# Kernel tuning notes

Hardware: AMD Instinct MI355X
Metric: run time of the kernel (lower is better)

## Reference

```python
import jax, jax.numpy as jnp
import numpy as np

G = 4          # groups
K = 3          # kernel_size
INC = 64       # channels


def conv3x3(x, w):
    # x: (B, Cin, H, W), w: (Cout, Cin, 3, 3), stride 1, pad 1, no bias
    return jax.lax.conv_general_dilated(
        x, w, window_strides=(1, 1), padding=[(1, 1), (1, 1)],
        dimension_numbers=("NCHW", "OIHW", "NCHW"))


def pconv(x, w):
    # partial conv: 3x3 conv on first C//4 channels, rest untouched
    dc = x.shape[1] // 4
    x1 = conv3x3(x[:, :dc], w)
    return jnp.concatenate([x1, x[:, dc:]], axis=1)


def conv1x1(x, w, b):
    # w: (Cout, Cin), b: (Cout,)
    return jnp.einsum("bchw,oc->bohw", x, w) + b[None, :, None, None]


def deform_sample(img, offset, mask_sig, dilation):
    """Modulated deformable sampling (DSMv3): for each output pixel and each of
    the K*K kernel taps, bilinearly sample img at p + dilated_tap + offset and
    modulate by the (sigmoided) mask. Returns (B, Cg, K*K, H, W)."""
    b, cg, H, W = img.shape
    K2 = K * K
    off = offset.reshape(b, K2, 2, H, W)  # (dy, dx) per tap
    ky = jnp.repeat(jnp.arange(K), K).astype(img.dtype)   # (K2,) row of tap
    kx = jnp.tile(jnp.arange(K), K).astype(img.dtype)     # (K2,) col of tap
    # padding = center*dilation so sampling grid is centered: p = i + (k-1)*dil
    base_y = jnp.arange(H, dtype=img.dtype)[None, :, None] + ((ky - 1.0) * dilation)[:, None, None]  # (K2,H,1)
    base_x = jnp.arange(W, dtype=img.dtype)[None, None, :] + ((kx - 1.0) * dilation)[:, None, None]  # (K2,1,W)
    py = base_y[None] + off[:, :, 0]  # (B,K2,H,W)
    px = base_x[None] + off[:, :, 1]  # (B,K2,H,W)

    y0 = jnp.floor(py)
    x0 = jnp.floor(px)
    wy = py - y0
    wx = px - x0
    imgf = img.reshape(b, cg, H * W)

    def corner(yi, xi, wgt):
        valid = ((yi >= 0) & (yi <= H - 1) & (xi >= 0) & (xi <= W - 1)).astype(img.dtype)
        yc = jnp.clip(yi, 0, H - 1).astype(jnp.int32)
        xc = jnp.clip(xi, 0, W - 1).astype(jnp.int32)
        flat = (yc * W + xc).reshape(b, 1, -1)  # (B,1,K2*H*W)
        v = jnp.take_along_axis(imgf, flat, axis=2).reshape(b, cg, K2, H, W)
        return v * (wgt * valid).reshape(b, 1, K2, H, W)

    val = (corner(y0, x0, (1 - wy) * (1 - wx))
           + corner(y0, x0 + 1, (1 - wy) * wx)
           + corner(y0 + 1, x0, wy * (1 - wx))
           + corner(y0 + 1, x0 + 1, wy * wx))
    return val * mask_sig[:, None]  # (B,Cg,K2,H,W)


def setup_inputs() -> dict:
    key = jax.random.key(0)
    ks = jax.random.split(key, 8)
    dc = INC // 4
    x = jax.random.normal(ks[0], (4, INC, 128, 128), dtype=jnp.float32)
    y = jax.random.normal(ks[1], (8, INC, 128, 128), dtype=jnp.float32)
    # learned params (small random so offsets stay near-zero, as after training warmup)
    offset_pconv_w = jax.random.normal(ks[2], (G, dc, dc, 3, 3), dtype=jnp.float32) * 0.1
    offset_w = jax.random.normal(ks[3], (G, 2 * K * K, INC), dtype=jnp.float32) * 0.1
    offset_b = jax.random.normal(ks[4], (G, 2 * K * K), dtype=jnp.float32) * 0.1
    mask_pconv_w = jax.random.normal(ks[5], (dc, dc, 3, 3), dtype=jnp.float32) * 0.1
    mask_w = jax.random.normal(ks[6], (K * K, INC), dtype=jnp.float32) * 0.1
    mask_b = jax.random.normal(ks[7], (K * K,), dtype=jnp.float32) * 0.1
    return {"x": x, "y": y,
            "offset_pconv_w": offset_pconv_w, "offset_w": offset_w, "offset_b": offset_b,
            "mask_pconv_w": mask_pconv_w, "mask_w": mask_w, "mask_b": mask_b}


def reference(x, y, offset_pconv_w, offset_w, offset_b, mask_pconv_w, mask_w, mask_b):
    b, c, h, w = x.shape
    cg = c // G
    mask = jax.nn.sigmoid(conv1x1(pconv(x, mask_pconv_w), mask_w, mask_b))  # (B,K2,H,W), shared
    y1, y2 = jnp.split(y, 2, axis=0)
    outs1, outs2 = [], []
    for g in range(G):
        offset = conv1x1(pconv(x, offset_pconv_w[g]), offset_w[g], offset_b[g])  # (B,2*K2,H,W)
        dil = 2 * g + 1
        outs1.append(deform_sample(y1[:, g * cg:(g + 1) * cg], offset, mask, dil))
        outs2.append(deform_sample(y2[:, g * cg:(g + 1) * cg], offset, mask, dil))
    y1n = jnp.concatenate(outs1, axis=1)  # (B,C,K2,H,W)
    y2n = jnp.concatenate(outs2, axis=1)
    return jnp.concatenate([y1n, y2n], axis=0)  # (2B,C,K2,H,W)
```

## Files before the change

### kernel.cpp

```cpp
#include <hip/hip_runtime.h>
#include <hip/hip_bf16.h>
#include <math.h>

constexpr int HH   = 128;
constexpr int WW   = 128;
constexpr int HWsz = HH * WW;

constexpr long OFFS_OFF = 0;
constexpr long MASK_OFF = OFFS_OFF + 4L * 4 * 18 * HWsz;
constexpr long WEO_OFF  = MASK_OFF + 4L * 9 * HWsz;
constexpr long WRO_OFF  = WEO_OFF + 4L * 16 * 9 * 18;
constexpr long WEM_OFF  = WRO_OFF + 4L * 48 * 18;
constexpr long WRM_OFF  = WEM_OFF + 16L * 9 * 9;
constexpr long YT_OFF   = WRM_OFF + 48L * 9;

__global__ __launch_bounds__(256) void prep_kernel(
    const float* __restrict__ off_pw,
    const float* __restrict__ off_w,
    const float* __restrict__ mask_pw,
    const float* __restrict__ mask_w,
    float* __restrict__ Weff_off, float* __restrict__ Wraw_off,
    float* __restrict__ Weff_mask, float* __restrict__ Wraw_mask)
{
    const int i = blockIdx.x * 256 + threadIdx.x;
    if (i < 10368) {
        const int o = i % 18; int r = i / 18;
        const int t = r % 9;  r /= 9;
        const int ci = r % 16; const int g = r / 16;
        float s = 0.f;
        for (int co = 0; co < 16; ++co)
            s += off_w[(g * 18 + o) * 64 + co] *
                 off_pw[((g * 16 + co) * 16 + ci) * 9 + t];
        Weff_off[i] = s;
    } else if (i < 10368 + 3456) {
        const int j = i - 10368;
        const int o = j % 18; int r = j / 18;
        const int c = r % 48; const int g = r / 48;
        Wraw_off[j] = off_w[(g * 18 + o) * 64 + 16 + c];
    } else if (i < 10368 + 3456 + 1296) {
        const int j = i - 13824;
        const int o = j % 9; int r = j / 9;
        const int t = r % 9; const int ci = r / 9;
        float s = 0.f;
        for (int co = 0; co < 16; ++co)
            s += mask_w[o * 64 + co] * mask_pw[((co * 16) + ci) * 9 + t];
        Weff_mask[j] = s;
    } else if (i < 10368 + 3456 + 1296 + 432) {
        const int j = i - 15120;
        const int o = j % 9; const int c = j / 9;
        Wraw_mask[j] = mask_w[o * 64 + 16 + c];
    }
}

__global__ __launch_bounds__(256) void transpose_kernel(
    const float* __restrict__ y, float* __restrict__ yT)
{
    __shared__ __align__(16) float tile[256][20];
    const int t  = threadIdx.x;
    const int by = blockIdx.y;
    const int tile_base = blockIdx.x * 256;
    #pragma unroll
    for (int ci = 0; ci < 16; ++ci)
        tile[t][ci] = y[(long)(by * 16 + ci) * HWsz + tile_base + t];
    __syncthreads();
    float* dst = yT + ((long)by * HWsz + tile_base) * 16;
    #pragma unroll
    for (int pass = 0; pass < 4; ++pass) {
        const int j = pass * 1024 + t * 4;
        const int px = j >> 4, ci = j & 15;
        *reinterpret_cast<float4*>(dst + j) =
            *reinterpret_cast<const float4*>(&tile[px][ci]);
    }
}

__global__ __launch_bounds__(256) void field_kernel(
    const float* __restrict__ x,
    const float* __restrict__ Weff_off, const float* __restrict__ Wraw_off,
    const float* __restrict__ off_b,
    const float* __restrict__ Weff_mask, const float* __restrict__ Wraw_mask,
    const float* __restrict__ mask_b,
    float* __restrict__ offs, float* __restrict__ maskf)
{
    const int p    = blockIdx.x * 256 + threadIdx.x;
    const int bx   = blockIdx.y;
    const int pass = blockIdx.z;
    const int h = p >> 7, w = p & 127;
    const float* xb = x + (long)bx * 64 * HWsz;

    if (pass < 4) {
        const int g = pass;
        float acc[18];
        #pragma unroll
        for (int o = 0; o < 18; ++o) acc[o] = off_b[g * 18 + o];
        for (int ci = 0; ci < 16; ++ci) {
            const float* xp = xb + ci * HWsz;
            #pragma unroll
            for (int t = 0; t < 9; ++t) {
                const int hh = h + t / 3 - 1, w2 = w + t % 3 - 1;
                float xv = 0.f;
                if ((unsigned)hh < 128u && (unsigned)w2 < 128u)
                    xv = xp[hh * 128 + w2];
                const float* wp = Weff_off + ((g * 16 + ci) * 9 + t) * 18;
                #pragma unroll
                for (int o = 0; o < 18; ++o) acc[o] = fmaf(xv, wp[o], acc[o]);
            }
        }
        for (int c = 0; c < 48; ++c) {
            const float xv = xb[(16 + c) * HWsz + p];
            const float* wp = Wraw_off + (g * 48 + c) * 18;
            #pragma unroll
            for (int o = 0; o < 18; ++o) acc[o] = fmaf(xv, wp[o], acc[o]);
        }
        float* op = offs + ((long)(bx * 4 + g) * 18) * HWsz + p;
        #pragma unroll
        for (int o = 0; o < 18; ++o) op[(long)o * HWsz] = acc[o];
    } else {
        float acc[9];
        #pragma unroll
        for (int o = 0; o < 9; ++o) acc[o] = mask_b[o];
        for (int ci = 0; ci < 16; ++ci) {
            const float* xp = xb + ci * HWsz;
            #pragma unroll
            for (int t = 0; t < 9; ++t) {
                const int hh = h + t / 3 - 1, w2 = w + t % 3 - 1;
                float xv = 0.f;
                if ((unsigned)hh < 128u && (unsigned)w2 < 128u)
                    xv = xp[hh * 128 + w2];
                const float* wp = Weff_mask + (ci * 9 + t) * 9;
                #pragma unroll
                for (int o = 0; o < 9; ++o) acc[o] = fmaf(xv, wp[o], acc[o]);
            }
        }
        for (int c = 0; c < 48; ++c) {
            const float xv = xb[(16 + c) * HWsz + p];
            const float* wp = Wraw_mask + c * 9;
            #pragma unroll
            for (int o = 0; o < 9; ++o) acc[o] = fmaf(xv, wp[o], acc[o]);
        }
        float* op = maskf + (long)bx * 9 * HWsz + p;
        #pragma unroll
        for (int o = 0; o < 9; ++o)
            op[(long)o * HWsz] = 1.0f / (1.0f + __expf(-acc[o]));
    }
}

__global__ __launch_bounds__(256) void sample_kernel(
    const float* __restrict__ yT,
    const float* __restrict__ offs,
    const float* __restrict__ maskf,
    float* __restrict__ out)
{
    const int p  = blockIdx.x * 256 + threadIdx.x;
    const int bg = blockIdx.y;
    const int bx = bg >> 2, g = bg & 3;
    const int k  = blockIdx.z;
    const int h = p >> 7, w = p & 127;
    const int dil = 2 * g + 1;

    const long obase = ((long)(bx * 4 + g) * 18) * HWsz + p;
    const float dy = offs[obase + (long)(2 * k) * HWsz];
    const float dx = offs[obase + (long)(2 * k + 1) * HWsz];
    const float m  = maskf[((long)bx * 9 + k) * HWsz + p];

    const float py = (float)(h + (k / 3 - 1) * dil) + dy;
    const float px = (float)(w + (k % 3 - 1) * dil) + dx;
    const float y0f = floorf(py), x0f = floorf(px);
    const float wy = py - y0f, wx = px - x0f;
    const int y0 = (int)y0f, x0 = (int)x0f;

    const bool vy0 = (unsigned)y0 < 128u, vy1 = (unsigned)(y0 + 1) < 128u;
    const int  yc0 = min(max(y0, 0), 127), yc1 = min(max(y0 + 1, 0), 127);
    const float r0 = vy0 ? (1.f - wy) * m : 0.f;
    const float r1 = vy1 ? wy * m : 0.f;

    const int  c0 = min(max(x0, 0), 126);
    const bool interior = (x0 >= 0) & (x0 <= 126);
    float b0, b1;
    if (interior)        { b0 = 1.f - wx; b1 = wx; }
    else if (x0 == -1)   { b0 = wx;       b1 = 0.f; }
    else if (x0 == 127)  { b0 = 0.f;      b1 = 1.f - wx; }
    else                 { b0 = 0.f;      b1 = 0.f; }
    const float w00 = r0 * b0, w01 = r0 * b1;
    const float w10 = r1 * b0, w11 = r1 * b1;

    const long off0 = ((long)yc0 * 128 + c0) * 16;
    const long off1 = ((long)yc1 * 128 + c0) * 16;
    const long ostride = 9L * HWsz;

    #pragma unroll
    for (int half = 0; half < 2; ++half) {
        const float* base = yT + (long)((bx + half * 4) * 4 + g) * (HWsz * 16L);
        const float4* A0 = reinterpret_cast<const float4*>(base + off0);
        const float4* A1 = reinterpret_cast<const float4*>(base + off1);

        float acc[16];
        float4 q[8];
        #pragma unroll
        for (int j = 0; j < 8; ++j) q[j] = A0[j];
        #pragma unroll
        for (int ci = 0; ci < 16; ++ci) {
            const float vA = reinterpret_cast<const float*>(q)[ci];
            const float vB = reinterpret_cast<const float*>(q)[16 + ci];
            acc[ci] = fmaf(vA, w00, vB * w01);
        }
        #pragma unroll
        for (int j = 0; j < 8; ++j) q[j] = A1[j];
        float* op = out + ((long)((bx + half * 4) * 64 + g * 16) * 9 + k) * HWsz + p;
        #pragma unroll
        for (int ci = 0; ci < 16; ++ci) {
            const float vA = reinterpret_cast<const float*>(q)[ci];
            const float vB = reinterpret_cast<const float*>(q)[16 + ci];
            op[(long)ci * ostride] = fmaf(vA, w10, fmaf(vB, w11, acc[ci]));
        }
    }
}

extern "C" void kernel_launch(void* const* d_in, const int* in_sizes, int n_in,
                              void* d_out, int out_size, void* d_ws, size_t ws_size,
                              hipStream_t stream) {
    const float* x       = (const float*)d_in[0];
    const float* y       = (const float*)d_in[1];
    const float* off_pw  = (const float*)d_in[2];
    const float* off_w   = (const float*)d_in[3];
    const float* off_b   = (const float*)d_in[4];
    const float* mask_pw = (const float*)d_in[5];
    const float* mask_w  = (const float*)d_in[6];
    const float* mask_b  = (const float*)d_in[7];
    float* out = (float*)d_out;

    float* ws        = (float*)d_ws;
    float* offs      = ws + OFFS_OFF;
    float* maskf     = ws + MASK_OFF;
    float* Weff_off  = ws + WEO_OFF;
    float* Wraw_off  = ws + WRO_OFF;
    float* Weff_mask = ws + WEM_OFF;
    float* Wraw_mask = ws + WRM_OFF;
    float* yT        = ws + YT_OFF;

    prep_kernel<<<61, 256, 0, stream>>>(off_pw, off_w, mask_pw, mask_w,
                                        Weff_off, Wraw_off, Weff_mask, Wraw_mask);
    transpose_kernel<<<dim3(64, 32), 256, 0, stream>>>(y, yT);
    field_kernel<<<dim3(64, 4, 5), 256, 0, stream>>>(
        x, Weff_off, Wraw_off, off_b, Weff_mask, Wraw_mask, mask_b, offs, maskf);
    sample_kernel<<<dim3(64, 16, 9), 256, 0, stream>>>(yT, offs, maskf, out);
}
```

Before: 511.5 us.

## Stage field weights in LDS, two pixels per thread, split sample channels across four lanes

The field kernel now stages the per-group effective weights in shared memory, padded to float4 rows. Each thread computes two pixels 64 rows apart, so every weight read is reused twice and the grid is halved. The sample kernel now gives each pixel to four lanes, each handling four channels with float4 loads. This cuts registers per thread and raises parallelism, at the cost of redundant offset/mask loads and bilinear weight math in each lane, plus a larger grid.

```diff
diff --git a/kernel.cpp b/kernel.cpp
--- a/kernel.cpp
+++ b/kernel.cpp
@@ -81,7 +81,9 @@
     const float* __restrict__ mask_b,
     float* __restrict__ offs, float* __restrict__ maskf)
 {
-    const int p    = blockIdx.x * 256 + threadIdx.x;
+    __shared__ __align__(16) float wlds[3840];
+    const int tid  = threadIdx.x;
+    const int p    = blockIdx.x * 256 + tid;
     const int bx   = blockIdx.y;
     const int pass = blockIdx.z;
     const int h = p >> 7, w = p & 127;
@@ -89,58 +91,147 @@
 
     if (pass < 4) {
         const int g = pass;
-        float acc[18];
+        for (int i = tid; i < 2880; i += 256) {
+            const int o = i % 20;
+            float v = 0.f;
+            if (o < 18) {
+                const int t = (i / 20) % 9, ci = i / 180;
+                v = Weff_off[((g * 16 + ci) * 9 + t) * 18 + o];
+            }
+            wlds[i] = v;
+        }
+        for (int i = tid; i < 960; i += 256) {
+            const int o = i % 20, c = i / 20;
+            wlds[2880 + i] = (o < 18) ? Wraw_off[(g * 48 + c) * 18 + o] : 0.f;
+        }
+        __syncthreads();
+
+        float acc0[20], acc1[20];
         #pragma unroll
-        for (int o = 0; o < 18; ++o) acc[o] = off_b[g * 18 + o];
+        for (int o = 0; o < 20; ++o) {
+            const float b = (o < 18) ? off_b[g * 18 + o] : 0.f;
+            acc0[o] = b; acc1[o] = b;
+        }
         for (int ci = 0; ci < 16; ++ci) {
             const float* xp = xb + ci * HWsz;
             #pragma unroll
             for (int t = 0; t < 9; ++t) {
-                const int hh = h + t / 3 - 1, w2 = w + t % 3 - 1;
-                float xv = 0.f;
-                if ((unsigned)hh < 128u && (unsigned)w2 < 128u)
-                    xv = xp[hh * 128 + w2];
-                const float* wp = Weff_off + ((g * 16 + ci) * 9 + t) * 18;
+                const int hh0 = h + t / 3 - 1, w2 = w + t % 3 - 1;
+                const int hh1 = hh0 + 64;
+                float xv0 = 0.f, xv1 = 0.f;
+                if ((unsigned)w2 < 128u) {
+                    if ((unsigned)hh0 < 128u) xv0 = xp[hh0 * 128 + w2];
+                    if ((unsigned)hh1 < 128u) xv1 = xp[hh1 * 128 + w2];
+                }
+                const float4* wq = reinterpret_cast<const float4*>(&wlds[(ci * 9 + t) * 20]);
                 #pragma unroll
-                for (int o = 0; o < 18; ++o) acc[o] = fmaf(xv, wp[o], acc[o]);
+                for (int q = 0; q < 5; ++q) {
+                    const float4 wv = wq[q];
+                    acc0[q*4+0] = fmaf(xv0, wv.x, acc0[q*4+0]);
+                    acc0[q*4+1] = fmaf(xv0, wv.y, acc0[q*4+1]);
+                    acc0[q*4+2] = fmaf(xv0, wv.z, acc0[q*4+2]);
+                    acc0[q*4+3] = fmaf(xv0, wv.w, acc0[q*4+3]);
+                    acc1[q*4+0] = fmaf(xv1, wv.x, acc1[q*4+0]);
+                    acc1[q*4+1] = fmaf(xv1, wv.y, acc1[q*4+1]);
+                    acc1[q*4+2] = fmaf(xv1, wv.z, acc1[q*4+2]);
+                    acc1[q*4+3] = fmaf(xv1, wv.w, acc1[q*4+3]);
+                }
             }
         }
         for (int c = 0; c < 48; ++c) {
-            const float xv = xb[(16 + c) * HWsz + p];
-            const float* wp = Wraw_off + (g * 48 + c) * 18;
+            const float xv0 = xb[(16 + c) * HWsz + p];
+            const float xv1 = xb[(16 + c) * HWsz + p + 8192];
+            const float4* wq = reinterpret_cast<const float4*>(&wlds[2880 + c * 20]);
             #pragma unroll
-            for (int o = 0; o < 18; ++o) acc[o] = fmaf(xv, wp[o], acc[o]);
+            for (int q = 0; q < 5; ++q) {
+                const float4 wv = wq[q];
+                acc0[q*4+0] = fmaf(xv0, wv.x, acc0[q*4+0]);
+                acc0[q*4+1] = fmaf(xv0, wv.y, acc0[q*4+1]);
+                acc0[q*4+2] = fmaf(xv0, wv.z, acc0[q*4+2]);
+                acc0[q*4+3] = fmaf(xv0, wv.w, acc0[q*4+3]);
+                acc1[q*4+0] = fmaf(xv1, wv.x, acc1[q*4+0]);
+                acc1[q*4+1] = fmaf(xv1, wv.y, acc1[q*4+1]);
+                acc1[q*4+2] = fmaf(xv1, wv.z, acc1[q*4+2]);
+                acc1[q*4+3] = fmaf(xv1, wv.w, acc1[q*4+3]);
+            }
         }
         float* op = offs + ((long)(bx * 4 + g) * 18) * HWsz + p;
         #pragma unroll
-        for (int o = 0; o < 18; ++o) op[(long)o * HWsz] = acc[o];
+        for (int o = 0; o < 18; ++o) {
+            op[(long)o * HWsz]        = acc0[o];
+            op[(long)o * HWsz + 8192] = acc1[o];
+        }
     } else {
-        float acc[9];
+        for (int i = tid; i < 1728; i += 256) {
+            const int o = i % 12;
+            float v = 0.f;
+            if (o < 9) {
+                const int t = (i / 12) % 9, ci = i / 108;
+                v = Weff_mask[(ci * 9 + t) * 9 + o];
+            }
+            wlds[i] = v;
+        }
+        for (int i = tid; i < 576; i += 256) {
+            const int o = i % 12, c = i / 12;
+            wlds[1728 + i] = (o < 9) ? Wraw_mask[c * 9 + o] : 0.f;
+        }
+        __syncthreads();
+
+        float acc0[12], acc1[12];
         #pragma unroll
-        for (int o = 0; o < 9; ++o) acc[o] = mask_b[o];
+        for (int o = 0; o < 12; ++o) {
+            const float b = (o < 9) ? mask_b[o] : 0.f;
+            acc0[o] = b; acc1[o] = b;
+        }
         for (int ci = 0; ci < 16; ++ci) {
             const float* xp = xb + ci * HWsz;
             #pragma unroll
             for (int t = 0; t < 9; ++t) {
-                const int hh = h + t / 3 - 1, w2 = w + t % 3 - 1;
-                float xv = 0.f;
-                if ((unsigned)hh < 128u && (unsigned)w2 < 128u)
-                    xv = xp[hh * 128 + w2];
-                const float* wp = Weff_mask + (ci * 9 + t) * 9;
+                const int hh0 = h + t / 3 - 1, w2 = w + t % 3 - 1;
+                const int hh1 = hh0 + 64;
+                float xv0 = 0.f, xv1 = 0.f;
+                if ((unsigned)w2 < 128u) {
+                    if ((unsigned)hh0 < 128u) xv0 = xp[hh0 * 128 + w2];
+                    if ((unsigned)hh1 < 128u) xv1 = xp[hh1 * 128 + w2];
+                }
+                const float4* wq = reinterpret_cast<const float4*>(&wlds[(ci * 9 + t) * 12]);
                 #pragma unroll
-                for (int o = 0; o < 9; ++o) acc[o] = fmaf(xv, wp[o], acc[o]);
+                for (int q = 0; q < 3; ++q) {
+                    const float4 wv = wq[q];
+                    acc0[q*4+0] = fmaf(xv0, wv.x, acc0[q*4+0]);
+                    acc0[q*4+1] = fmaf(xv0, wv.y, acc0[q*4+1]);
+                    acc0[q*4+2] = fmaf(xv0, wv.z, acc0[q*4+2]);
+                    acc0[q*4+3] = fmaf(xv0, wv.w, acc0[q*4+3]);
+                    acc1[q*4+0] = fmaf(xv1, wv.x, acc1[q*4+0]);
+                    acc1[q*4+1] = fmaf(xv1, wv.y, acc1[q*4+1]);
+                    acc1[q*4+2] = fmaf(xv1, wv.z, acc1[q*4+2]);
+                    acc1[q*4+3] = fmaf(xv1, wv.w, acc1[q*4+3]);
+                }
             }
         }
         for (int c = 0; c < 48; ++c) {
-            const float xv = xb[(16 + c) * HWsz + p];
-            const float* wp = Wraw_mask + c * 9;
+            const float xv0 = xb[(16 + c) * HWsz + p];
+            const float xv1 = xb[(16 + c) * HWsz + p + 8192];
+            const float4* wq = reinterpret_cast<const float4*>(&wlds[1728 + c * 12]);
             #pragma unroll
-            for (int o = 0; o < 9; ++o) acc[o] = fmaf(xv, wp[o], acc[o]);
+            for (int q = 0; q < 3; ++q) {
+                const float4 wv = wq[q];
+                acc0[q*4+0] = fmaf(xv0, wv.x, acc0[q*4+0]);
+                acc0[q*4+1] = fmaf(xv0, wv.y, acc0[q*4+1]);
+                acc0[q*4+2] = fmaf(xv0, wv.z, acc0[q*4+2]);
+                acc0[q*4+3] = fmaf(xv0, wv.w, acc0[q*4+3]);
+                acc1[q*4+0] = fmaf(xv1, wv.x, acc1[q*4+0]);
+                acc1[q*4+1] = fmaf(xv1, wv.y, acc1[q*4+1]);
+                acc1[q*4+2] = fmaf(xv1, wv.z, acc1[q*4+2]);
+                acc1[q*4+3] = fmaf(xv1, wv.w, acc1[q*4+3]);
+            }
         }
         float* op = maskf + (long)bx * 9 * HWsz + p;
         #pragma unroll
-        for (int o = 0; o < 9; ++o)
-            op[(long)o * HWsz] = 1.0f / (1.0f + __expf(-acc[o]));
+        for (int o = 0; o < 9; ++o) {
+            op[(long)o * HWsz]        = 1.0f / (1.0f + __expf(-acc0[o]));
+            op[(long)o * HWsz + 8192] = 1.0f / (1.0f + __expf(-acc1[o]));
+        }
     }
 }
 
@@ -150,7 +241,9 @@
     const float* __restrict__ maskf,
     float* __restrict__ out)
 {
-    const int p  = blockIdx.x * 256 + threadIdx.x;
+    const int tid  = threadIdx.x;
+    const int quad = tid & 3;
+    const int p    = blockIdx.x * 64 + (tid >> 2);
     const int bg = blockIdx.y;
     const int bx = bg >> 2, g = bg & 3;
     const int k  = blockIdx.z;
@@ -183,35 +276,21 @@
     const float w00 = r0 * b0, w01 = r0 * b1;
     const float w10 = r1 * b0, w11 = r1 * b1;
 
-    const long off0 = ((long)yc0 * 128 + c0) * 16;
-    const long off1 = ((long)yc1 * 128 + c0) * 16;
-    const long ostride = 9L * HWsz;
+    const long off0 = ((long)yc0 * 128 + c0) * 16 + quad * 4;
+    const long off1 = ((long)yc1 * 128 + c0) * 16 + quad * 4;
 
     #pragma unroll
     for (int half = 0; half < 2; ++half) {
         const float* base = yT + (long)((bx + half * 4) * 4 + g) * (HWsz * 16L);
-        const float4* A0 = reinterpret_cast<const float4*>(base + off0);
-        const float4* A1 = reinterpret_cast<const float4*>(base + off1);
-
-        float acc[16];
-        float4 q[8];
-        #pragma unroll
-        for (int j = 0; j < 8; ++j) q[j] = A0[j];
-        #pragma unroll
-        for (int ci = 0; ci < 16; ++ci) {
-            const float vA = reinterpret_cast<const float*>(q)[ci];
-            const float vB = reinterpret_cast<const float*>(q)[16 + ci];
-            acc[ci] = fmaf(vA, w00, vB * w01);
-        }
-        #pragma unroll
-        for (int j = 0; j < 8; ++j) q[j] = A1[j];
-        float* op = out + ((long)((bx + half * 4) * 64 + g * 16) * 9 + k) * HWsz + p;
-        #pragma unroll
-        for (int ci = 0; ci < 16; ++ci) {
-            const float vA = reinterpret_cast<const float*>(q)[ci];
-            const float vB = reinterpret_cast<const float*>(q)[16 + ci];
-            op[(long)ci * ostride] = fmaf(vA, w10, fmaf(vB, w11, acc[ci]));
-        }
+        const float4 r0a = *reinterpret_cast<const float4*>(base + off0);
+        const float4 r0b = *reinterpret_cast<const float4*>(base + off0 + 16);
+        const float4 r1a = *reinterpret_cast<const float4*>(base + off1);
+        const float4 r1b = *reinterpret_cast<const float4*>(base + off1 + 16);
+        float* op = out + ((long)((bx + half * 4) * 64 + g * 16 + quad * 4) * 9 + k) * HWsz + p;
+        op[0]            = fmaf(r0a.x, w00, fmaf(r0b.x, w01, fmaf(r1a.x, w10, r1b.x * w11)));
+        op[9L * HWsz]    = fmaf(r0a.y, w00, fmaf(r0b.y, w01, fmaf(r1a.y, w10, r1b.y * w11)));
+        op[18L * HWsz]   = fmaf(r0a.z, w00, fmaf(r0b.z, w01, fmaf(r1a.z, w10, r1b.z * w11)));
+        op[27L * HWsz]   = fmaf(r0a.w, w00, fmaf(r0b.w, w01, fmaf(r1a.w, w10, r1b.w * w11)));
     }
 }
 
@@ -240,7 +319,7 @@
     prep_kernel<<<61, 256, 0, stream>>>(off_pw, off_w, mask_pw, mask_w,
                                         Weff_off, Wraw_off, Weff_mask, Wraw_mask);
     transpose_kernel<<<dim3(64, 32), 256, 0, stream>>>(y, yT);
-    field_kernel<<<dim3(64, 4, 5), 256, 0, stream>>>(
+    field_kernel<<<dim3(32, 4, 5), 256, 0, stream>>>(
         x, Weff_off, Wraw_off, off_b, Weff_mask, Wraw_mask, mask_b, offs, maskf);
-    sample_kernel<<<dim3(64, 16, 9), 256, 0, stream>>>(yT, offs, maskf, out);
-}
+    sample_kernel<<<dim3(256, 16, 9), 256, 0, stream>>>(yT, offs, maskf, out);
+}
```

Result: slower. 569.1 us (+11.3%).

## Split sample channels across four threads per pixel and vectorize field weight loads

Applied to the files above, without the earlier changes.

The sample kernel now assigns four threads to each pixel, with each thread handling four of the sixteen channels. This cuts per-thread register use and load volume and raises parallelism, at the cost of recomputing the offset and bilinear weights four times and writing to output with a stride of four lanes per pixel. The field kernel's weight tables are padded to 20 and 12 entries per row so each tap can be read with float4 loads instead of scalar loads. This adds a few dead FMAs on the zero padding.

```diff
diff --git a/kernel.cpp b/kernel.cpp
--- a/kernel.cpp
+++ b/kernel.cpp
@@ -9,10 +9,10 @@
 constexpr long OFFS_OFF = 0;
 constexpr long MASK_OFF = OFFS_OFF + 4L * 4 * 18 * HWsz;
 constexpr long WEO_OFF  = MASK_OFF + 4L * 9 * HWsz;
-constexpr long WRO_OFF  = WEO_OFF + 4L * 16 * 9 * 18;
-constexpr long WEM_OFF  = WRO_OFF + 4L * 48 * 18;
-constexpr long WRM_OFF  = WEM_OFF + 16L * 9 * 9;
-constexpr long YT_OFF   = WRM_OFF + 48L * 9;
+constexpr long WRO_OFF  = WEO_OFF + 4L * 16 * 9 * 20;
+constexpr long WEM_OFF  = WRO_OFF + 4L * 48 * 20;
+constexpr long WRM_OFF  = WEM_OFF + 16L * 9 * 12;
+constexpr long YT_OFF   = WRM_OFF + 48L * 12;
 
 __global__ __launch_bounds__(256) void prep_kernel(
     const float* __restrict__ off_pw,
@@ -23,32 +23,34 @@
     float* __restrict__ Weff_mask, float* __restrict__ Wraw_mask)
 {
     const int i = blockIdx.x * 256 + threadIdx.x;
-    if (i < 10368) {
-        const int o = i % 18; int r = i / 18;
+    if (i < 11520) {
+        const int o = i % 20; int r = i / 20;
         const int t = r % 9;  r /= 9;
         const int ci = r % 16; const int g = r / 16;
         float s = 0.f;
-        for (int co = 0; co < 16; ++co)
-            s += off_w[(g * 18 + o) * 64 + co] *
-                 off_pw[((g * 16 + co) * 16 + ci) * 9 + t];
+        if (o < 18)
+            for (int co = 0; co < 16; ++co)
+                s += off_w[(g * 18 + o) * 64 + co] *
+                     off_pw[((g * 16 + co) * 16 + ci) * 9 + t];
         Weff_off[i] = s;
-    } else if (i < 10368 + 3456) {
-        const int j = i - 10368;
-        const int o = j % 18; int r = j / 18;
+    } else if (i < 11520 + 3840) {
+        const int j = i - 11520;
+        const int o = j % 20; int r = j / 20;
         const int c = r % 48; const int g = r / 48;
-        Wraw_off[j] = off_w[(g * 18 + o) * 64 + 16 + c];
-    } else if (i < 10368 + 3456 + 1296) {
-        const int j = i - 13824;
-        const int o = j % 9; int r = j / 9;
+        Wraw_off[j] = (o < 18) ? off_w[(g * 18 + o) * 64 + 16 + c] : 0.f;
+    } else if (i < 11520 + 3840 + 1728) {
+        const int j = i - 15360;
+        const int o = j % 12; int r = j / 12;
         const int t = r % 9; const int ci = r / 9;
         float s = 0.f;
-        for (int co = 0; co < 16; ++co)
-            s += mask_w[o * 64 + co] * mask_pw[((co * 16) + ci) * 9 + t];
+        if (o < 9)
+            for (int co = 0; co < 16; ++co)
+                s += mask_w[o * 64 + co] * mask_pw[((co * 16) + ci) * 9 + t];
         Weff_mask[j] = s;
-    } else if (i < 10368 + 3456 + 1296 + 432) {
-        const int j = i - 15120;
-        const int o = j % 9; const int c = j / 9;
-        Wraw_mask[j] = mask_w[o * 64 + 16 + c];
+    } else if (i < 11520 + 3840 + 1728 + 576) {
+        const int j = i - 17088;
+        const int o = j % 12; const int c = j / 12;
+        Wraw_mask[j] = (o < 9) ? mask_w[o * 64 + 16 + c] : 0.f;
     }
 }
 
@@ -89,9 +91,9 @@
 
     if (pass < 4) {
         const int g = pass;
-        float acc[18];
-        #pragma unroll
-        for (int o = 0; o < 18; ++o) acc[o] = off_b[g * 18 + o];
+        float acc[20];
+        #pragma unroll
+        for (int o = 0; o < 20; ++o) acc[o] = (o < 18) ? off_b[g * 18 + o] : 0.f;
         for (int ci = 0; ci < 16; ++ci) {
             const float* xp = xb + ci * HWsz;
             #pragma unroll
@@ -100,24 +102,38 @@
                 float xv = 0.f;
                 if ((unsigned)hh < 128u && (unsigned)w2 < 128u)
                     xv = xp[hh * 128 + w2];
-                const float* wp = Weff_off + ((g * 16 + ci) * 9 + t) * 18;
+                const float4* wq = reinterpret_cast<const float4*>(
+                    Weff_off + ((g * 16 + ci) * 9 + t) * 20);
                 #pragma unroll
-                for (int o = 0; o < 18; ++o) acc[o] = fmaf(xv, wp[o], acc[o]);
+                for (int q = 0; q < 5; ++q) {
+                    const float4 wv = wq[q];
+                    acc[q*4+0] = fmaf(xv, wv.x, acc[q*4+0]);
+                    acc[q*4+1] = fmaf(xv, wv.y, acc[q*4+1]);
+                    acc[q*4+2] = fmaf(xv, wv.z, acc[q*4+2]);
+                    acc[q*4+3] = fmaf(xv, wv.w, acc[q*4+3]);
+                }
             }
         }
         for (int c = 0; c < 48; ++c) {
             const float xv = xb[(16 + c) * HWsz + p];
-            const float* wp = Wraw_off + (g * 48 + c) * 18;
-            #pragma unroll
-            for (int o = 0; o < 18; ++o) acc[o] = fmaf(xv, wp[o], acc[o]);
+            const float4* wq = reinterpret_cast<const float4*>(
+                Wraw_off + (g * 48 + c) * 20);
+            #pragma unroll
+            for (int q = 0; q < 5; ++q) {
+                const float4 wv = wq[q];
+                acc[q*4+0] = fmaf(xv, wv.x, acc[q*4+0]);
+                acc[q*4+1] = fmaf(xv, wv.y, acc[q*4+1]);
+                acc[q*4+2] = fmaf(xv, wv.z, acc[q*4+2]);
+                acc[q*4+3] = fmaf(xv, wv.w, acc[q*4+3]);
+            }
         }
         float* op = offs + ((long)(bx * 4 + g) * 18) * HWsz + p;
         #pragma unroll
         for (int o = 0; o < 18; ++o) op[(long)o * HWsz] = acc[o];
     } else {
-        float acc[9];
-        #pragma unroll
-        for (int o = 0; o < 9; ++o) acc[o] = mask_b[o];
+        float acc[12];
+        #pragma unroll
+        for (int o = 0; o < 12; ++o) acc[o] = (o < 9) ? mask_b[o] : 0.f;
         for (int ci = 0; ci < 16; ++ci) {
             const float* xp = xb + ci * HWsz;
             #pragma unroll
@@ -126,16 +142,29 @@
                 float xv = 0.f;
                 if ((unsigned)hh < 128u && (unsigned)w2 < 128u)
                     xv = xp[hh * 128 + w2];
-                const float* wp = Weff_mask + (ci * 9 + t) * 9;
+                const float4* wq = reinterpret_cast<const float4*>(
+                    Weff_mask + (ci * 9 + t) * 12);
                 #pragma unroll
-                for (int o = 0; o < 9; ++o) acc[o] = fmaf(xv, wp[o], acc[o]);
+                for (int q = 0; q < 3; ++q) {
+                    const float4 wv = wq[q];
+                    acc[q*4+0] = fmaf(xv, wv.x, acc[q*4+0]);
+                    acc[q*4+1] = fmaf(xv, wv.y, acc[q*4+1]);
+                    acc[q*4+2] = fmaf(xv, wv.z, acc[q*4+2]);
+                    acc[q*4+3] = fmaf(xv, wv.w, acc[q*4+3]);
+                }
             }
         }
         for (int c = 0; c < 48; ++c) {
             const float xv = xb[(16 + c) * HWsz + p];
-            const float* wp = Wraw_mask + c * 9;
-            #pragma unroll
-            for (int o = 0; o < 9; ++o) acc[o] = fmaf(xv, wp[o], acc[o]);
+            const float4* wq = reinterpret_cast<const float4*>(Wraw_mask + c * 12);
+            #pragma unroll
+            for (int q = 0; q < 3; ++q) {
+                const float4 wv = wq[q];
+                acc[q*4+0] = fmaf(xv, wv.x, acc[q*4+0]);
+                acc[q*4+1] = fmaf(xv, wv.y, acc[q*4+1]);
+                acc[q*4+2] = fmaf(xv, wv.z, acc[q*4+2]);
+                acc[q*4+3] = fmaf(xv, wv.w, acc[q*4+3]);
+            }
         }
         float* op = maskf + (long)bx * 9 * HWsz + p;
         #pragma unroll
@@ -150,7 +179,9 @@
     const float* __restrict__ maskf,
     float* __restrict__ out)
 {
-    const int p  = blockIdx.x * 256 + threadIdx.x;
+    const int tid  = threadIdx.x;
+    const int quad = tid & 3;
+    const int p    = blockIdx.x * 64 + (tid >> 2);
     const int bg = blockIdx.y;
     const int bx = bg >> 2, g = bg & 3;
     const int k  = blockIdx.z;
@@ -183,35 +214,21 @@
     const float w00 = r0 * b0, w01 = r0 * b1;
     const float w10 = r1 * b0, w11 = r1 * b1;
 
-    const long off0 = ((long)yc0 * 128 + c0) * 16;
-    const long off1 = ((long)yc1 * 128 + c0) * 16;
-    const long ostride = 9L * HWsz;
+    const long off0 = ((long)yc0 * 128 + c0) * 16 + quad * 4;
+    const long off1 = ((long)yc1 * 128 + c0) * 16 + quad * 4;
 
     #pragma unroll
     for (int half = 0; half < 2; ++half) {
         const float* base = yT + (long)((bx + half * 4) * 4 + g) * (HWsz * 16L);
-        const float4* A0 = reinterpret_cast<const float4*>(base + off0);
-        const float4* A1 = reinterpret_cast<const float4*>(base + off1);
-
-        float acc[16];
-        float4 q[8];
-        #pragma unroll
-        for (int j = 0; j < 8; ++j) q[j] = A0[j];
-        #pragma unroll
-        for (int ci = 0; ci < 16; ++ci) {
-            const float vA = reinterpret_cast<const float*>(q)[ci];
-            const float vB = reinterpret_cast<const float*>(q)[16 + ci];
-            acc[ci] = fmaf(vA, w00, vB * w01);
-        }
-        #pragma unroll
-        for (int j = 0; j < 8; ++j) q[j] = A1[j];
-        float* op = out + ((long)((bx + half * 4) * 64 + g * 16) * 9 + k) * HWsz + p;
-        #pragma unroll
-        for (int ci = 0; ci < 16; ++ci) {
-            const float vA = reinterpret_cast<const float*>(q)[ci];
-            const float vB = reinterpret_cast<const float*>(q)[16 + ci];
-            op[(long)ci * ostride] = fmaf(vA, w10, fmaf(vB, w11, acc[ci]));
-        }
+        const float4 r0a = *reinterpret_cast<const float4*>(base + off0);
+        const float4 r0b = *reinterpret_cast<const float4*>(base + off0 + 16);
+        const float4 r1a = *reinterpret_cast<const float4*>(base + off1);
+        const float4 r1b = *reinterpret_cast<const float4*>(base + off1 + 16);
+        float* op = out + ((long)((bx + half * 4) * 64 + g * 16 + quad * 4) * 9 + k) * HWsz + p;
+        op[0]            = fmaf(r0a.x, w00, fmaf(r0b.x, w01, fmaf(r1a.x, w10, r1b.x * w11)));
+        op[9L * HWsz]    = fmaf(r0a.y, w00, fmaf(r0b.y, w01, fmaf(r1a.y, w10, r1b.y * w11)));
+        op[18L * HWsz]   = fmaf(r0a.z, w00, fmaf(r0b.z, w01, fmaf(r1a.z, w10, r1b.z * w11)));
+        op[27L * HWsz]   = fmaf(r0a.w, w00, fmaf(r0b.w, w01, fmaf(r1a.w, w10, r1b.w * w11)));
     }
 }
 
@@ -237,10 +254,10 @@
     float* Wraw_mask = ws + WRM_OFF;
     float* yT        = ws + YT_OFF;
 
-    prep_kernel<<<61, 256, 0, stream>>>(off_pw, off_w, mask_pw, mask_w,
+    prep_kernel<<<69, 256, 0, stream>>>(off_pw, off_w, mask_pw, mask_w,
                                         Weff_off, Wraw_off, Weff_mask, Wraw_mask);
     transpose_kernel<<<dim3(64, 32), 256, 0, stream>>>(y, yT);
     field_kernel<<<dim3(64, 4, 5), 256, 0, stream>>>(
         x, Weff_off, Wraw_off, off_b, Weff_mask, Wraw_mask, mask_b, offs, maskf);
-    sample_kernel<<<dim3(64, 16, 9), 256, 0, stream>>>(yT, offs, maskf, out);
-}
+    sample_kernel<<<dim3(256, 16, 9), 256, 0, stream>>>(yT, offs, maskf, out);
+}
```

Result: slower. 545.2 us (+6.6%).
